# Performance work log

Measured on AMD Instinct MI355X. Metric: run time of the kernel, lower is better.

## Reference

```python
import jax, jax.numpy as jnp
import numpy as np
import math

B, QL, HID = 4, 4, 4096          # batch, speculative q_len, hidden_size
NH, NKV, HD = 32, 8, 128         # attention heads, kv heads, head_dim
GROUPS = NH // NKV               # GQA repeat factor = 4
PRIOR = 4096                     # cached (prior) KV length
THETA = 1.0e6                    # Mixtral rope_theta


def setup_inputs() -> dict:
    key = jax.random.key(0)
    ks = jax.random.split(key, 7)
    hidden_states = jax.random.normal(ks[0], (B, QL, HID), jnp.float32)
    past_k = jax.random.normal(ks[1], (B, NKV, PRIOR, HD), jnp.float32)
    past_v = jax.random.normal(ks[2], (B, NKV, PRIOR, HD), jnp.float32)
    wq = jax.random.normal(ks[3], (HID, NH * HD), jnp.float32) * 0.02
    wk = jax.random.normal(ks[4], (HID, NKV * HD), jnp.float32) * 0.02
    wv = jax.random.normal(ks[5], (HID, NKV * HD), jnp.float32) * 0.02
    wo = jax.random.normal(ks[6], (NH * HD, HID), jnp.float32) * 0.02
    # prior mask: all cached positions visible
    attention_mask = jnp.ones((B, 1, QL, PRIOR), dtype=bool)
    # active mask: causal over the speculative window
    active_mask = jnp.broadcast_to(jnp.tril(jnp.ones((QL, QL), dtype=bool)), (B, 1, QL, QL))
    position_ids = jnp.broadcast_to(PRIOR + jnp.arange(QL, dtype=jnp.int64), (B, QL))
    return {"hidden_states": hidden_states, "past_k": past_k, "past_v": past_v,
            "wq": wq, "wk": wk, "wv": wv, "wo": wo,
            "attention_mask": attention_mask, "active_mask": active_mask,
            "position_ids": position_ids}


def _rotate_half(x):
    x1, x2 = jnp.split(x, 2, axis=-1)
    return jnp.concatenate([-x2, x1], axis=-1)


def _rope_cos_sin(position_ids):
    inv_freq = 1.0 / (THETA ** (jnp.arange(0, HD, 2, dtype=jnp.float32) / HD))  # [HD/2]
    freqs = position_ids.astype(jnp.float32)[..., None] * inv_freq              # [B,QL,HD/2]
    emb = jnp.concatenate([freqs, freqs], axis=-1)                              # [B,QL,HD]
    return jnp.cos(emb)[:, None], jnp.sin(emb)[:, None]                          # [B,1,QL,HD]


def reference(hidden_states, past_k, past_v, wq, wk, wv, wo,
              attention_mask, active_mask, position_ids):
    # fused QKV projection (no bias in Mixtral)
    q = (hidden_states @ wq).reshape(B, QL, NH, HD).transpose(0, 2, 1, 3)   # [B,NH,QL,HD]
    k = (hidden_states @ wk).reshape(B, QL, NKV, HD).transpose(0, 2, 1, 3)  # [B,NKV,QL,HD]
    v = (hidden_states @ wv).reshape(B, QL, NKV, HD).transpose(0, 2, 1, 3)
    # RoPE on Q and active K
    cos, sin = _rope_cos_sin(position_ids)
    q = q * cos + _rotate_half(q) * sin
    k = k * cos + _rotate_half(k) * sin
    # GQA repeat_kv
    k_prior = jnp.repeat(past_k, GROUPS, axis=1)  # [B,NH,PRIOR,HD]
    v_prior = jnp.repeat(past_v, GROUPS, axis=1)
    k_active = jnp.repeat(k, GROUPS, axis=1)      # [B,NH,QL,HD]
    v_active = jnp.repeat(v, GROUPS, axis=1)
    scale = 1.0 / math.sqrt(HD)
    neg = jnp.finfo(jnp.float32).min
    prior_scores = jnp.einsum('bhqd,bhkd->bhqk', q, k_prior) * scale
    prior_scores = jnp.where(attention_mask, prior_scores, neg)
    active_scores = jnp.einsum('bhqd,bhkd->bhqk', q, k_active) * scale
    active_scores = jnp.where(active_mask, active_scores, neg)   # is_speculation=True
    # decomposed softmax: shared max and shared divisor across prior/active
    max_score = jnp.maximum(prior_scores.max(-1, keepdims=True),
                            active_scores.max(-1, keepdims=True))
    prior_exp = jnp.exp(prior_scores - max_score)
    active_exp = jnp.exp(active_scores - max_score)
    divisor = prior_exp.sum(-1, keepdims=True) + active_exp.sum(-1, keepdims=True)
    attn = (jnp.einsum('bhqk,bhkd->bhqd', prior_exp / divisor, v_prior) +
            jnp.einsum('bhqk,bhkd->bhqd', active_exp / divisor, v_active))
    attn = attn.transpose(0, 2, 1, 3).reshape(B, QL, NH * HD)
    return attn @ wo
```

## Files before the change

### kernel.cpp

```cpp
#include <hip/hip_runtime.h>
#include <math.h>

#define NROWS 16
#define NCOLS 6144
#define HID   4096
#define NKV   8
#define HD    128
#define PRIOR 4096
#define NCH   32
#define CHUNK 128
#define SUB   64
#define KCQ   64
#define NKCQ  64
#define KCO   64
#define NKCO  64

__device__ __forceinline__ float rdlane(float v, int l) {
    return __int_as_float(__builtin_amdgcn_readlane(__float_as_int(v), l));
}

__global__ __launch_bounds__(128)
void k_qkv_partial(const float* __restrict__ hid,
                   const float* __restrict__ wq,
                   const float* __restrict__ wk,
                   const float* __restrict__ wv,
                   float* __restrict__ part)
{
    const int t   = threadIdx.x;
    const int col = blockIdx.x * 256 + t * 2;
    const int kc  = blockIdx.y;
    const int k0  = kc * KCQ;
    const float* w; int wn, wcol;
    if (col < 4096)      { w = wq; wn = 4096; wcol = col; }
    else if (col < 5120) { w = wk; wn = 1024; wcol = col - 4096; }
    else                 { w = wv; wn = 1024; wcol = col - 5120; }
    const float* wp = w + wcol + (size_t)k0 * wn;

    float acc[NROWS][2];
#pragma unroll
    for (int m = 0; m < NROWS; m++) { acc[m][0] = 0.f; acc[m][1] = 0.f; }
#pragma unroll 4
    for (int kk = 0; kk < KCQ; kk += 4) {
        const float2 w0 = *(const float2*)(wp + (size_t)(kk + 0) * wn);
        const float2 w1 = *(const float2*)(wp + (size_t)(kk + 1) * wn);
        const float2 w2 = *(const float2*)(wp + (size_t)(kk + 2) * wn);
        const float2 w3 = *(const float2*)(wp + (size_t)(kk + 3) * wn);
#pragma unroll
        for (int m = 0; m < NROWS; m++) {
            const float4 h4 = *(const float4*)(hid + (size_t)m * HID + k0 + kk);
            acc[m][0] = fmaf(h4.x, w0.x, fmaf(h4.y, w1.x, fmaf(h4.z, w2.x, fmaf(h4.w, w3.x, acc[m][0]))));
            acc[m][1] = fmaf(h4.x, w0.y, fmaf(h4.y, w1.y, fmaf(h4.z, w2.y, fmaf(h4.w, w3.y, acc[m][1]))));
        }
    }
    float* po = part + (size_t)kc * (NROWS * NCOLS) + col;
#pragma unroll
    for (int m = 0; m < NROWS; m++)
        *(float2*)(po + (size_t)m * NCOLS) = make_float2(acc[m][0], acc[m][1]);
}

__global__ __launch_bounds__(256)
void k_reduce_rope(const float* __restrict__ part, float* __restrict__ qkv)
{
    const int tid  = blockIdx.x * 256 + threadIdx.x;
    const int w    = tid >> 6, lane = tid & 63;
    const int u    = w * 16 + (lane & 15);
    const int sub  = lane >> 4;
    const int cs   = sub * 16;
    const double L64 = 0.21586735246819178;

    if (u < 32768) {
        const int d = u & 63, h = (u >> 6) & 31, r = u >> 11;
        const int c1 = h * HD + d;
        float s1 = 0.f, s2 = 0.f;
#pragma unroll 8
        for (int i = 0; i < 16; i++) {
            const float* p = part + (size_t)(cs + i) * (NROWS * NCOLS) + r * NCOLS + c1;
            s1 += p[0]; s2 += p[64];
        }
        s1 += __shfl_xor(s1, 16); s1 += __shfl_xor(s1, 32);
        s2 += __shfl_xor(s2, 16); s2 += __shfl_xor(s2, 32);
        if (sub == 0) {
            const double ang = (double)(PRIOR + (r & 3)) * exp(-(double)d * L64);
            double sv, cv; sincos(ang, &sv, &cv);
            const float cf = (float)cv, sf = (float)sv, sc = 0.08838834764831845f;
            qkv[r * NCOLS + c1]      = (s1 * cf - s2 * sf) * sc;
            qkv[r * NCOLS + c1 + 64] = (s2 * cf + s1 * sf) * sc;
        }
    } else if (u < 40960) {
        const int idx = u - 32768;
        const int d = idx & 63, kh = (idx >> 6) & 7, r = idx >> 9;
        const int c1 = 4096 + kh * HD + d;
        float s1 = 0.f, s2 = 0.f;
#pragma unroll 8
        for (int i = 0; i < 16; i++) {
            const float* p = part + (size_t)(cs + i) * (NROWS * NCOLS) + r * NCOLS + c1;
            s1 += p[0]; s2 += p[64];
        }
        s1 += __shfl_xor(s1, 16); s1 += __shfl_xor(s1, 32);
        s2 += __shfl_xor(s2, 16); s2 += __shfl_xor(s2, 32);
        if (sub == 0) {
            const double ang = (double)(PRIOR + (r & 3)) * exp(-(double)d * L64);
            double sv, cv; sincos(ang, &sv, &cv);
            const float cf = (float)cv, sf = (float)sv;
            qkv[r * NCOLS + c1]      = s1 * cf - s2 * sf;
            qkv[r * NCOLS + c1 + 64] = s2 * cf + s1 * sf;
        }
    } else {
        const int idx = u - 40960;
        const int n = idx & 1023, r = idx >> 10;
        const int c1 = 5120 + n;
        float s = 0.f;
#pragma unroll 8
        for (int i = 0; i < 16; i++)
            s += part[(size_t)(cs + i) * (NROWS * NCOLS) + r * NCOLS + c1];
        s += __shfl_xor(s, 16); s += __shfl_xor(s, 32);
        if (sub == 0) qkv[r * NCOLS + c1] = s;
    }
}

__global__ __launch_bounds__(256, 4)
void k_attn_prior(const float* __restrict__ qkv,
                  const float* __restrict__ pk,
                  const float* __restrict__ pv,
                  float* __restrict__ part3)
{
    const int chunk = blockIdx.x, kvh = blockIdx.y, b = blockIdx.z;
    const int t = threadIdx.x;
    const int lane = t & 63;

    __shared__ float kT[128][64];
    __shared__ float qT[128][16];

    const int qt = t >> 6;
    const int h  = (lane >> 4) & 3;
    const int kt = lane & 15;

    const size_t kvoff = ((size_t)(b * NKV + kvh) * PRIOR + (size_t)chunk * CHUNK) * HD;
    const float* kbase = pk + kvoff;
    const float* vbase = pv + kvoff;

    float4 kreg[8];
    {
        const float* kr = kbase + (size_t)lane * HD + qt * 32;
#pragma unroll
        for (int i = 0; i < 8; i++) kreg[i] = *(const float4*)(kr + i * 4);
    }

    for (int i = t; i < 2048; i += 256) {
        const int r = i & 15, d = i >> 4;
        const int ql = r & 3, g = r >> 2;
        qT[d][r] = qkv[(size_t)(b * 4 + ql) * NCOLS + (kvh * 4 + g) * HD + d];
    }

    float m_r[4], l_r[4], o[4][2];
#pragma unroll
    for (int i = 0; i < 4; i++) { m_r[i] = -INFINITY; l_r[i] = 0.f; o[i][0] = 0.f; o[i][1] = 0.f; }

    for (int st = 0; st < CHUNK / SUB; st++) {
#pragma unroll
        for (int i = 0; i < 8; i++) {
            const int d = qt * 32 + i * 4;
            kT[d + 0][lane] = kreg[i].x; kT[d + 1][lane] = kreg[i].y;
            kT[d + 2][lane] = kreg[i].z; kT[d + 3][lane] = kreg[i].w;
        }
        if (st == 0) {
            const float* kr = kbase + (size_t)(SUB + lane) * HD + qt * 32;
#pragma unroll
            for (int i = 0; i < 8; i++) kreg[i] = *(const float4*)(kr + i * 4);
        }
        __syncthreads();

        float a[4][4];
#pragma unroll
        for (int i = 0; i < 4; i++)
#pragma unroll
            for (int j = 0; j < 4; j++) a[i][j] = 0.f;
#pragma unroll 4
        for (int dd = 0; dd < 32; dd++) {
            const int d = h * 32 + dd;
            const float4 q4 = *(const float4*)(&qT[d][qt * 4]);
            const float4 k4 = *(const float4*)(&kT[d][kt * 4]);
            a[0][0]=fmaf(q4.x,k4.x,a[0][0]); a[0][1]=fmaf(q4.x,k4.y,a[0][1]); a[0][2]=fmaf(q4.x,k4.z,a[0][2]); a[0][3]=fmaf(q4.x,k4.w,a[0][3]);
            a[1][0]=fmaf(q4.y,k4.x,a[1][0]); a[1][1]=fmaf(q4.y,k4.y,a[1][1]); a[1][2]=fmaf(q4.y,k4.z,a[1][2]); a[1][3]=fmaf(q4.y,k4.w,a[1][3]);
            a[2][0]=fmaf(q4.z,k4.x,a[2][0]); a[2][1]=fmaf(q4.z,k4.y,a[2][1]); a[2][2]=fmaf(q4.z,k4.z,a[2][2]); a[2][3]=fmaf(q4.z,k4.w,a[2][3]);
            a[3][0]=fmaf(q4.w,k4.x,a[3][0]); a[3][1]=fmaf(q4.w,k4.y,a[3][1]); a[3][2]=fmaf(q4.w,k4.z,a[3][2]); a[3][3]=fmaf(q4.w,k4.w,a[3][3]);
        }
        __syncthreads();

        const float* vs = vbase + (size_t)st * SUB * HD + (lane << 1);
        float2 vb[4][4];
#pragma unroll
        for (int g = 0; g < 4; ++g)
#pragma unroll
            for (int j = 0; j < 4; ++j)
                vb[g][j] = *(const float2*)(vs + (size_t)(g * 4 + j) * HD);

#pragma unroll
        for (int i = 0; i < 4; i++)
#pragma unroll
            for (int j = 0; j < 4; j++) {
                float v = a[i][j];
                v += __shfl_xor(v, 16);
                v += __shfl_xor(v, 32);
                a[i][j] = v;
            }
        float al[4], pr[4][4];
#pragma unroll
        for (int i = 0; i < 4; i++) {
            float mx = fmaxf(fmaxf(a[i][0], a[i][1]), fmaxf(a[i][2], a[i][3]));
            mx = fmaxf(mx, __shfl_xor(mx, 1));
            mx = fmaxf(mx, __shfl_xor(mx, 2));
            mx = fmaxf(mx, __shfl_xor(mx, 4));
            mx = fmaxf(mx, __shfl_xor(mx, 8));
            const float mn = fmaxf(m_r[i], mx);
            al[i] = __expf(m_r[i] - mn);
            m_r[i] = mn;
            float s = 0.f;
#pragma unroll
            for (int j = 0; j < 4; j++) { pr[i][j] = __expf(a[i][j] - mn); s += pr[i][j]; }
            s += __shfl_xor(s, 1); s += __shfl_xor(s, 2);
            s += __shfl_xor(s, 4); s += __shfl_xor(s, 8);
            l_r[i] = l_r[i] * al[i] + s;
        }
#pragma unroll
        for (int i = 0; i < 4; i++) { o[i][0] *= al[i]; o[i][1] *= al[i]; }

#pragma unroll
        for (int g4 = 0; g4 < 16; ++g4) {
            const float2 v0 = vb[g4 & 3][0];
            const float2 v1 = vb[g4 & 3][1];
            const float2 v2 = vb[g4 & 3][2];
            const float2 v3 = vb[g4 & 3][3];
            if (g4 < 12) {
#pragma unroll
                for (int j = 0; j < 4; ++j)
                    vb[g4 & 3][j] = *(const float2*)(vs + (size_t)((g4 + 4) * 4 + j) * HD);
            }
#pragma unroll
            for (int i = 0; i < 4; i++) {
                const float p0 = rdlane(pr[i][0], g4);
                const float p1 = rdlane(pr[i][1], g4);
                const float p2 = rdlane(pr[i][2], g4);
                const float p3v = rdlane(pr[i][3], g4);
                o[i][0] = fmaf(p0,  v0.x, o[i][0]); o[i][1] = fmaf(p0,  v0.y, o[i][1]);
                o[i][0] = fmaf(p1,  v1.x, o[i][0]); o[i][1] = fmaf(p1,  v1.y, o[i][1]);
                o[i][0] = fmaf(p2,  v2.x, o[i][0]); o[i][1] = fmaf(p2,  v2.y, o[i][1]);
                o[i][0] = fmaf(p3v, v3.x, o[i][0]); o[i][1] = fmaf(p3v, v3.y, o[i][1]);
            }
        }
    }

    float* pout = part3 + (size_t)((b * NKV + kvh) * NCH + chunk) * 2080;
    if (lane == 0) {
#pragma unroll
        for (int i = 0; i < 4; i++) { pout[qt * 4 + i] = m_r[i]; pout[16 + qt * 4 + i] = l_r[i]; }
    }
#pragma unroll
    for (int i = 0; i < 4; i++)
        *(float2*)(pout + 32 + (size_t)(qt * 4 + i) * HD + (lane << 1)) =
            make_float2(o[i][0], o[i][1]);
}

__global__ __launch_bounds__(128)
void k_combine(const float* __restrict__ qkv,
               const float* __restrict__ part3,
               float* __restrict__ attn)
{
    const int bid = blockIdx.x;
    const int hr = bid & 1, g = (bid >> 1) & 3, kvh = (bid >> 3) & 7, b = bid >> 6;
    const int t = threadIdx.x;
    const int lr0 = hr * 2, lr1 = lr0 + 1;
    __shared__ float qL[2][128], kA[4][128], vA[4][128];
    __shared__ float mC[NCH][2], lC[NCH][2], fC[NCH][2];
    __shared__ float sAct[2][4], pA[2][4], invL[2];

    for (int i = t; i < 256; i += 128) {
        const int lrl = i >> 7, d = i & 127;
        qL[lrl][d] = qkv[(size_t)(b * 4 + lr0 + lrl) * NCOLS + (kvh * 4 + g) * HD + d];
    }
    for (int i = t; i < 512; i += 128) {
        const int ql = i >> 7, d = i & 127;
        kA[ql][d] = qkv[(size_t)(b * 4 + ql) * NCOLS + 4096 + kvh * HD + d];
        vA[ql][d] = qkv[(size_t)(b * 4 + ql) * NCOLS + 5120 + kvh * HD + d];
    }
    const float* p3 = part3 + (size_t)(b * NKV + kvh) * NCH * 2080;
    for (int i = t; i < NCH * 2; i += 128) {
        const int c = i >> 1, lrl = i & 1;
        mC[c][lrl] = p3[c * 2080 + g * 4 + lr0 + lrl];
        lC[c][lrl] = p3[c * 2080 + 16 + g * 4 + lr0 + lrl];
    }
    __syncthreads();
    if (t < 64) {
        const int pp = t >> 3, dd = t & 7;
        const int lrl = pp >> 2, k = pp & 3;
        float s = 0.f;
#pragma unroll
        for (int d = 0; d < 16; d++)
            s = fmaf(qL[lrl][dd * 16 + d], kA[k][dd * 16 + d], s);
        s += __shfl_xor(s, 1); s += __shfl_xor(s, 2); s += __shfl_xor(s, 4);
        if (dd == 0) sAct[lrl][k] = s;
    }
    __syncthreads();
    if (t < 64) {
        const int lrl = t >> 5, c = t & 31;
        const int lr = lr0 + lrl;
        const float m  = mC[c][lrl];
        const bool act = (c < 4) && (c <= lr);
        const float sa = act ? sAct[lrl][c] : -INFINITY;
        float M = fmaxf(m, sa);
        M = fmaxf(M, __shfl_xor(M, 1));
        M = fmaxf(M, __shfl_xor(M, 2));
        M = fmaxf(M, __shfl_xor(M, 4));
        M = fmaxf(M, __shfl_xor(M, 8));
        M = fmaxf(M, __shfl_xor(M, 16));
        const float f = __expf(m - M);
        fC[c][lrl] = f;
        const float pact = act ? __expf(sa - M) : 0.f;
        if (c < 4) pA[lrl][c] = pact;
        float l = fmaf(f, lC[c][lrl], pact);
        l += __shfl_xor(l, 1); l += __shfl_xor(l, 2);
        l += __shfl_xor(l, 4); l += __shfl_xor(l, 8); l += __shfl_xor(l, 16);
        if (c == 0) invL[lrl] = 1.f / l;
    }
    __syncthreads();

    const int d = t;
    float o0 = 0.f, o1 = 0.f;
#pragma unroll 4
    for (int c = 0; c < NCH; c++) {
        const float* pa = p3 + c * 2080 + 32 + (g * 4 + lr0) * HD + d;
        o0 = fmaf(fC[c][0], pa[0],  o0);
        o1 = fmaf(fC[c][1], pa[HD], o1);
    }
#pragma unroll
    for (int k = 0; k < 4; k++) {
        const float v = vA[k][d];
        o0 = fmaf(pA[0][k], v, o0);
        o1 = fmaf(pA[1][k], v, o1);
    }
    attn[(size_t)(b * 4 + lr0) * HID + (kvh * 4 + g) * HD + d] = o0 * invL[0];
    attn[(size_t)(b * 4 + lr1) * HID + (kvh * 4 + g) * HD + d] = o1 * invL[1];
}

__global__ __launch_bounds__(128)
void k_out_partial(const float* __restrict__ attn,
                   const float* __restrict__ wo,
                   float* __restrict__ part)
{
    const int t = threadIdx.x;
    const int col = blockIdx.x * 256 + t * 2;
    const int kc = blockIdx.y;
    const int k0 = kc * KCO;
    const float* wp = wo + col + (size_t)k0 * HID;

    float acc[NROWS][2];
#pragma unroll
    for (int m = 0; m < NROWS; m++) { acc[m][0] = 0.f; acc[m][1] = 0.f; }
#pragma unroll 4
    for (int kk = 0; kk < KCO; kk += 4) {
        const float2 w0 = *(const float2*)(wp + (size_t)(kk + 0) * HID);
        const float2 w1 = *(const float2*)(wp + (size_t)(kk + 1) * HID);
        const float2 w2 = *(const float2*)(wp + (size_t)(kk + 2) * HID);
        const float2 w3 = *(const float2*)(wp + (size_t)(kk + 3) * HID);
#pragma unroll
        for (int m = 0; m < NROWS; m++) {
            const float4 h4 = *(const float4*)(attn + (size_t)m * HID + k0 + kk);
            acc[m][0] = fmaf(h4.x, w0.x, fmaf(h4.y, w1.x, fmaf(h4.z, w2.x, fmaf(h4.w, w3.x, acc[m][0]))));
            acc[m][1] = fmaf(h4.x, w0.y, fmaf(h4.y, w1.y, fmaf(h4.z, w2.y, fmaf(h4.w, w3.y, acc[m][1]))));
        }
    }
    float* po = part + (size_t)kc * (NROWS * HID) + col;
#pragma unroll
    for (int m = 0; m < NROWS; m++)
        *(float2*)(po + (size_t)m * HID) = make_float2(acc[m][0], acc[m][1]);
}

__global__ __launch_bounds__(256)
void k_out_reduce(const float* __restrict__ part, float* __restrict__ out)
{
    const int tid = blockIdx.x * 256 + threadIdx.x;
    const int w = tid >> 6, lane = tid & 63;
    const int oid = w * 16 + (lane & 15);
    const int sub = lane >> 4;
    const float* p = part + (size_t)oid * 4 + (size_t)(sub * 16) * (NROWS * HID);
    float4 s = make_float4(0.f, 0.f, 0.f, 0.f);
#pragma unroll 8
    for (int c = 0; c < 16; c++) {
        const float4 a = *(const float4*)(p + (size_t)c * (NROWS * HID));
        s.x += a.x; s.y += a.y; s.z += a.z; s.w += a.w;
    }
    s.x += __shfl_xor(s.x, 16); s.x += __shfl_xor(s.x, 32);
    s.y += __shfl_xor(s.y, 16); s.y += __shfl_xor(s.y, 32);
    s.z += __shfl_xor(s.z, 16); s.z += __shfl_xor(s.z, 32);
    s.w += __shfl_xor(s.w, 16); s.w += __shfl_xor(s.w, 32);
    if (sub == 0) *(float4*)(out + (size_t)oid * 4) = s;
}

extern "C" void kernel_launch(void* const* d_in, const int* in_sizes, int n_in,
                              void* d_out, int out_size, void* d_ws, size_t ws_size,
                              hipStream_t stream)
{
    (void)in_sizes; (void)n_in; (void)out_size; (void)ws_size;
    const float* hid = (const float*)d_in[0];
    const float* pk  = (const float*)d_in[1];
    const float* pv  = (const float*)d_in[2];
    const float* wq  = (const float*)d_in[3];
    const float* wk  = (const float*)d_in[4];
    const float* wv  = (const float*)d_in[5];
    const float* wo  = (const float*)d_in[6];
    float* out = (float*)d_out;
    float* ws  = (float*)d_ws;

    float* P1   = ws;
    float* P3   = ws;
    float* P5   = ws;
    float* qkv  = ws + 6291456;
    float* attn = ws + 6389760;

    k_qkv_partial<<<dim3(24, NKCQ), 128, 0, stream>>>(hid, wq, wk, wv, P1);
    k_reduce_rope<<<896, 256, 0, stream>>>(P1, qkv);
    k_attn_prior<<<dim3(NCH, NKV, 4), 256, 0, stream>>>(qkv, pk, pv, P3);
    k_combine<<<256, 128, 0, stream>>>(qkv, P3, attn);
    k_out_partial<<<dim3(16, NKCO), 128, 0, stream>>>(attn, wo, P5);
    k_out_reduce<<<256, 256, 0, stream>>>(P5, out);
}
```

Measured before the change: 314.9 us.

## Halve prior-attention chunk size to double split-K parallelism

Splits the cached KV sequence into 64 chunks of 64 keys instead of 32 chunks of 128, so the prior-attention kernel launches twice as many blocks, and raises its occupancy hint to 6 blocks per CU. The K transpose tile, QK score tile, softmax and PV loops are reworked for 32-key sub-tiles, and the V loads are issued before the barrier so they overlap the QK compute. The combine kernel now merges 64 partial results per row with a wider shuffle reduction. In exchange, each block does less work per launch and the partial-result traffic and combine cost both double.

Measured after the change: 495.0 us. 57.2% more time.

```diff
diff --git a/kernel.cpp b/kernel.cpp
--- a/kernel.cpp
+++ b/kernel.cpp
@@ -7,9 +7,9 @@
 #define NKV   8
 #define HD    128
 #define PRIOR 4096
-#define NCH   32
-#define CHUNK 128
-#define SUB   64
+#define NCH   64
+#define CHUNK 64
+#define SUB   32
 #define KCQ   64
 #define NKCQ  64
 #define KCO   64
@@ -118,7 +118,7 @@
     }
 }
 
-__global__ __launch_bounds__(256, 4)
+__global__ __launch_bounds__(256, 6)
 void k_attn_prior(const float* __restrict__ qkv,
                   const float* __restrict__ pk,
                   const float* __restrict__ pv,
@@ -128,22 +128,25 @@
     const int t = threadIdx.x;
     const int lane = t & 63;
 
-    __shared__ float kT[128][64];
+    __shared__ float kT[128][32];
     __shared__ float qT[128][16];
 
     const int qt = t >> 6;
     const int h  = (lane >> 4) & 3;
     const int kt = lane & 15;
 
+    const int sk = lane & 31;
+    const int sd = (lane >> 5) * 16;
+
     const size_t kvoff = ((size_t)(b * NKV + kvh) * PRIOR + (size_t)chunk * CHUNK) * HD;
     const float* kbase = pk + kvoff;
     const float* vbase = pv + kvoff;
 
-    float4 kreg[8];
+    float4 kreg[4];
     {
-        const float* kr = kbase + (size_t)lane * HD + qt * 32;
-#pragma unroll
-        for (int i = 0; i < 8; i++) kreg[i] = *(const float4*)(kr + i * 4);
+        const float* kr = kbase + (size_t)sk * HD + qt * 32 + sd;
+#pragma unroll
+        for (int i = 0; i < 4; i++) kreg[i] = *(const float4*)(kr + i * 4);
     }
 
     for (int i = t; i < 2048; i += 256) {
@@ -157,57 +160,60 @@
     for (int i = 0; i < 4; i++) { m_r[i] = -INFINITY; l_r[i] = 0.f; o[i][0] = 0.f; o[i][1] = 0.f; }
 
     for (int st = 0; st < CHUNK / SUB; st++) {
-#pragma unroll
-        for (int i = 0; i < 8; i++) {
-            const int d = qt * 32 + i * 4;
-            kT[d + 0][lane] = kreg[i].x; kT[d + 1][lane] = kreg[i].y;
-            kT[d + 2][lane] = kreg[i].z; kT[d + 3][lane] = kreg[i].w;
+        {
+            const int d0 = qt * 32 + sd;
+#pragma unroll
+            for (int i = 0; i < 4; i++) {
+                kT[d0 + i * 4 + 0][sk] = kreg[i].x;
+                kT[d0 + i * 4 + 1][sk] = kreg[i].y;
+                kT[d0 + i * 4 + 2][sk] = kreg[i].z;
+                kT[d0 + i * 4 + 3][sk] = kreg[i].w;
+            }
         }
         if (st == 0) {
-            const float* kr = kbase + (size_t)(SUB + lane) * HD + qt * 32;
-#pragma unroll
-            for (int i = 0; i < 8; i++) kreg[i] = *(const float4*)(kr + i * 4);
-        }
+            const float* kr = kbase + (size_t)(SUB + sk) * HD + qt * 32 + sd;
+#pragma unroll
+            for (int i = 0; i < 4; i++) kreg[i] = *(const float4*)(kr + i * 4);
+        }
+
+        const float* vs = vbase + (size_t)st * SUB * HD + (lane << 1);
+        float2 vb[4][4];
+#pragma unroll
+        for (int g = 0; g < 4; ++g)
+#pragma unroll
+            for (int j = 0; j < 4; ++j)
+                vb[g][j] = *(const float2*)(vs + (size_t)(g * 4 + j) * HD);
+
         __syncthreads();
 
-        float a[4][4];
-#pragma unroll
-        for (int i = 0; i < 4; i++)
-#pragma unroll
-            for (int j = 0; j < 4; j++) a[i][j] = 0.f;
+        float a[4][2];
+#pragma unroll
+        for (int i = 0; i < 4; i++) { a[i][0] = 0.f; a[i][1] = 0.f; }
 #pragma unroll 4
         for (int dd = 0; dd < 32; dd++) {
             const int d = h * 32 + dd;
             const float4 q4 = *(const float4*)(&qT[d][qt * 4]);
-            const float4 k4 = *(const float4*)(&kT[d][kt * 4]);
-            a[0][0]=fmaf(q4.x,k4.x,a[0][0]); a[0][1]=fmaf(q4.x,k4.y,a[0][1]); a[0][2]=fmaf(q4.x,k4.z,a[0][2]); a[0][3]=fmaf(q4.x,k4.w,a[0][3]);
-            a[1][0]=fmaf(q4.y,k4.x,a[1][0]); a[1][1]=fmaf(q4.y,k4.y,a[1][1]); a[1][2]=fmaf(q4.y,k4.z,a[1][2]); a[1][3]=fmaf(q4.y,k4.w,a[1][3]);
-            a[2][0]=fmaf(q4.z,k4.x,a[2][0]); a[2][1]=fmaf(q4.z,k4.y,a[2][1]); a[2][2]=fmaf(q4.z,k4.z,a[2][2]); a[2][3]=fmaf(q4.z,k4.w,a[2][3]);
-            a[3][0]=fmaf(q4.w,k4.x,a[3][0]); a[3][1]=fmaf(q4.w,k4.y,a[3][1]); a[3][2]=fmaf(q4.w,k4.z,a[3][2]); a[3][3]=fmaf(q4.w,k4.w,a[3][3]);
+            const float2 k2 = *(const float2*)(&kT[d][kt * 2]);
+            a[0][0] = fmaf(q4.x, k2.x, a[0][0]); a[0][1] = fmaf(q4.x, k2.y, a[0][1]);
+            a[1][0] = fmaf(q4.y, k2.x, a[1][0]); a[1][1] = fmaf(q4.y, k2.y, a[1][1]);
+            a[2][0] = fmaf(q4.z, k2.x, a[2][0]); a[2][1] = fmaf(q4.z, k2.y, a[2][1]);
+            a[3][0] = fmaf(q4.w, k2.x, a[3][0]); a[3][1] = fmaf(q4.w, k2.y, a[3][1]);
         }
         __syncthreads();
 
-        const float* vs = vbase + (size_t)st * SUB * HD + (lane << 1);
-        float2 vb[4][4];
-#pragma unroll
-        for (int g = 0; g < 4; ++g)
-#pragma unroll
-            for (int j = 0; j < 4; ++j)
-                vb[g][j] = *(const float2*)(vs + (size_t)(g * 4 + j) * HD);
-
 #pragma unroll
         for (int i = 0; i < 4; i++)
 #pragma unroll
-            for (int j = 0; j < 4; j++) {
+            for (int j = 0; j < 2; j++) {
                 float v = a[i][j];
                 v += __shfl_xor(v, 16);
                 v += __shfl_xor(v, 32);
                 a[i][j] = v;
             }
-        float al[4], pr[4][4];
+        float al[4], pr[4][2];
 #pragma unroll
         for (int i = 0; i < 4; i++) {
-            float mx = fmaxf(fmaxf(a[i][0], a[i][1]), fmaxf(a[i][2], a[i][3]));
+            float mx = fmaxf(a[i][0], a[i][1]);
             mx = fmaxf(mx, __shfl_xor(mx, 1));
             mx = fmaxf(mx, __shfl_xor(mx, 2));
             mx = fmaxf(mx, __shfl_xor(mx, 4));
@@ -215,9 +221,9 @@
             const float mn = fmaxf(m_r[i], mx);
             al[i] = __expf(m_r[i] - mn);
             m_r[i] = mn;
-            float s = 0.f;
-#pragma unroll
-            for (int j = 0; j < 4; j++) { pr[i][j] = __expf(a[i][j] - mn); s += pr[i][j]; }
+            pr[i][0] = __expf(a[i][0] - mn);
+            pr[i][1] = __expf(a[i][1] - mn);
+            float s = pr[i][0] + pr[i][1];
             s += __shfl_xor(s, 1); s += __shfl_xor(s, 2);
             s += __shfl_xor(s, 4); s += __shfl_xor(s, 8);
             l_r[i] = l_r[i] * al[i] + s;
@@ -226,22 +232,22 @@
         for (int i = 0; i < 4; i++) { o[i][0] *= al[i]; o[i][1] *= al[i]; }
 
 #pragma unroll
-        for (int g4 = 0; g4 < 16; ++g4) {
+        for (int g4 = 0; g4 < 8; ++g4) {
             const float2 v0 = vb[g4 & 3][0];
             const float2 v1 = vb[g4 & 3][1];
             const float2 v2 = vb[g4 & 3][2];
             const float2 v3 = vb[g4 & 3][3];
-            if (g4 < 12) {
+            if (g4 < 4) {
 #pragma unroll
                 for (int j = 0; j < 4; ++j)
                     vb[g4 & 3][j] = *(const float2*)(vs + (size_t)((g4 + 4) * 4 + j) * HD);
             }
 #pragma unroll
             for (int i = 0; i < 4; i++) {
-                const float p0 = rdlane(pr[i][0], g4);
-                const float p1 = rdlane(pr[i][1], g4);
-                const float p2 = rdlane(pr[i][2], g4);
-                const float p3v = rdlane(pr[i][3], g4);
+                const float p0 = rdlane(pr[i][0], g4 * 2);
+                const float p1 = rdlane(pr[i][1], g4 * 2);
+                const float p2 = rdlane(pr[i][0], g4 * 2 + 1);
+                const float p3v = rdlane(pr[i][1], g4 * 2 + 1);
                 o[i][0] = fmaf(p0,  v0.x, o[i][0]); o[i][1] = fmaf(p0,  v0.y, o[i][1]);
                 o[i][0] = fmaf(p1,  v1.x, o[i][0]); o[i][1] = fmaf(p1,  v1.y, o[i][1]);
                 o[i][0] = fmaf(p2,  v2.x, o[i][0]); o[i][1] = fmaf(p2,  v2.y, o[i][1]);
@@ -301,8 +307,8 @@
         if (dd == 0) sAct[lrl][k] = s;
     }
     __syncthreads();
-    if (t < 64) {
-        const int lrl = t >> 5, c = t & 31;
+    {
+        const int lrl = t >> 6, c = t & 63;
         const int lr = lr0 + lrl;
         const float m  = mC[c][lrl];
         const bool act = (c < 4) && (c <= lr);
@@ -313,13 +319,14 @@
         M = fmaxf(M, __shfl_xor(M, 4));
         M = fmaxf(M, __shfl_xor(M, 8));
         M = fmaxf(M, __shfl_xor(M, 16));
+        M = fmaxf(M, __shfl_xor(M, 32));
         const float f = __expf(m - M);
         fC[c][lrl] = f;
         const float pact = act ? __expf(sa - M) : 0.f;
         if (c < 4) pA[lrl][c] = pact;
         float l = fmaf(f, lC[c][lrl], pact);
-        l += __shfl_xor(l, 1); l += __shfl_xor(l, 2);
-        l += __shfl_xor(l, 4); l += __shfl_xor(l, 8); l += __shfl_xor(l, 16);
+        l += __shfl_xor(l, 1); l += __shfl_xor(l, 2); l += __shfl_xor(l, 4);
+        l += __shfl_xor(l, 8); l += __shfl_xor(l, 16); l += __shfl_xor(l, 32);
         if (c == 0) invL[lrl] = 1.f / l;
     }
     __syncthreads();
```
